# Kernel tuning notes

Hardware: AMD Instinct MI355X
Metric: run time of the kernel (lower is better)

## Reference

```python
import jax, jax.numpy as jnp
import numpy as np

DIM = 1024
NUM_HEADS = 16
HEAD_DIM = DIM // NUM_HEADS
SCALE = HEAD_DIM ** -0.5


def setup_inputs() -> dict:
    key = jax.random.key(0)
    k1, k2, k3 = jax.random.split(key, 3)
    x = jax.random.normal(k1, (4, 2048, DIM), dtype=jnp.float32)
    w_qkv = jax.random.normal(k2, (DIM, 3 * DIM), dtype=jnp.float32) * (DIM ** -0.5)
    b_qkv = jnp.zeros((3 * DIM,), dtype=jnp.float32)
    w_proj = jax.random.normal(k3, (DIM, DIM), dtype=jnp.float32) * (DIM ** -0.5)
    b_proj = jnp.zeros((DIM,), dtype=jnp.float32)
    return {"x": x, "w_qkv": w_qkv, "b_qkv": b_qkv, "w_proj": w_proj, "b_proj": b_proj}


def reference(x, w_qkv, b_qkv, w_proj, b_proj):
    b, n, c = x.shape
    qkv = x @ w_qkv + b_qkv                       # [b, n, 3*dim]
    qkv = qkv.reshape(b, n, 3, NUM_HEADS, HEAD_DIM)
    qkv = jnp.transpose(qkv, (2, 0, 3, 1, 4))     # [3, b, H, n, hd]
    q, k, v = qkv[0], qkv[1], qkv[2]
    attn = jnp.einsum("bhqd,bhkd->bhqk", q, k) * SCALE
    attn = jax.nn.softmax(attn, axis=-1)
    out = jnp.einsum("bhqk,bhkd->bhqd", attn, v)  # [b, H, n, hd]
    out = jnp.transpose(out, (0, 2, 1, 3)).reshape(b, n, c)
    return out @ w_proj + b_proj
```

## Files before the change

### kernel.cpp

```cpp
#include <hip/hip_runtime.h>
#include <hip/hip_bf16.h>

typedef unsigned short u16;
typedef __attribute__((ext_vector_type(8))) short bf16x8;
typedef __attribute__((ext_vector_type(4))) float f32x4;
typedef __attribute__((ext_vector_type(16))) float f32x16;


__device__ __forceinline__ u16 f2bf(float f) {
  union { float f; unsigned u; } v; v.f = f;
  unsigned r = v.u + 0x7fffu + ((v.u >> 16) & 1u);
  return (u16)(r >> 16);
}

#if defined(__has_builtin)
#if __has_builtin(__builtin_amdgcn_cvt_pk_bf16_f32)
#define HAS_PK_BF16 1
#endif
#endif
__device__ __forceinline__ unsigned pk2bf(float a, float b) {
#ifdef HAS_PK_BF16
  typedef __attribute__((ext_vector_type(2))) __bf16 vbf2;
  union { vbf2 v; unsigned u; } u;
  u.v = __builtin_amdgcn_cvt_pk_bf16_f32(a, b);
  return u.u;
#else
  return (unsigned)f2bf(a) | ((unsigned)f2bf(b) << 16);
#endif
}

__device__ __forceinline__ f32x4 mfma16(bf16x8 a, bf16x8 b, f32x4 c) {
  return __builtin_amdgcn_mfma_f32_16x16x32_bf16(a, b, c, 0, 0, 0);
}
__device__ __forceinline__ f32x16 mfma32(bf16x8 a, bf16x8 b, f32x16 c) {
  return __builtin_amdgcn_mfma_f32_32x32x16_bf16(a, b, c, 0, 0, 0);
}

__device__ __forceinline__ void gl_lds16(const void* g, void* l) {
  __builtin_amdgcn_global_load_lds((__attribute__((address_space(1))) void*)g,
                                   (__attribute__((address_space(3))) void*)l,
                                   16, 0, 0);
}

__device__ __forceinline__ void stage128x32(const u16* g0, int ld, u16* lds) {
  const int t = threadIdx.x;
  const int wave = t >> 6;
#pragma unroll
  for (int j = 0; j < 2; ++j) {
    int c = j * 256 + t;
    const u16* gp = g0 + (size_t)(c >> 2) * ld + (c & 3) * 8;
    gl_lds16(gp, lds + (size_t)(j * 256 + wave * 64) * 8);
  }
}


__global__ void cvt_f32_bf16(const float* __restrict__ in, u16* __restrict__ out, int n) {
  int i = (blockIdx.x * blockDim.x + threadIdx.x) * 4;
  if (i >= n) return;
  float4 v = *(const float4*)(in + i);
  u16 o0 = f2bf(v.x), o1 = f2bf(v.y), o2 = f2bf(v.z), o3 = f2bf(v.w);
  ushort4 o; o.x = o0; o.y = o1; o.z = o2; o.w = o3;
  *(ushort4*)(out + i) = o;
}

__global__ void transpose_cvt(const float* __restrict__ in, u16* __restrict__ out,
                              int R, int C) {
  __shared__ u16 tile[64][65];
  int c0 = blockIdx.x * 64, r0 = blockIdx.y * 64;
  int lc = threadIdx.x & 63, lr = threadIdx.x >> 6;
#pragma unroll
  for (int i = 0; i < 16; ++i) {
    int r = lr + i * 4;
    tile[r][lc] = f2bf(in[(size_t)(r0 + r) * C + c0 + lc]);
  }
  __syncthreads();
#pragma unroll
  for (int i = 0; i < 16; ++i) {
    int c = lr + i * 4;
    out[(size_t)(c0 + c) * R + r0 + lc] = tile[lc][c];
  }
}

__global__ void transpose_v(const u16* __restrict__ Vb, u16* __restrict__ Vt) {
  __shared__ u16 tile[64][65];
  int bh = blockIdx.y;
  int s0 = blockIdx.x * 64;
  const u16* in = Vb + (size_t)bh * 2048 * 64;
  u16* out = Vt + (size_t)bh * 64 * 2048;
  int lc = threadIdx.x & 63, lr = threadIdx.x >> 6;
#pragma unroll
  for (int i = 0; i < 16; ++i) {
    int r = lr + i * 4;
    tile[r][lc] = in[(size_t)(s0 + r) * 64 + lc];
  }
  __syncthreads();
#pragma unroll
  for (int i = 0; i < 16; ++i) {
    int d = lr + i * 4;
    out[(size_t)d * 2048 + s0 + lc] = tile[lc][d];
  }
}


__global__ __launch_bounds__(256, 2) void gemm_qkv(
    const u16* __restrict__ A, const u16* __restrict__ Bt,
    const float* __restrict__ bias,
    u16* __restrict__ Qb, u16* __restrict__ Kb, u16* __restrict__ Vb) {
  __shared__ u16 As[128 * 32], Bs[128 * 32];
  const int row0 = blockIdx.x * 128, col0 = blockIdx.y * 128;
  const int t = threadIdx.x, lane = t & 63, wave = t >> 6;
  const int quad = lane >> 4, l15 = lane & 15;
  const int m_off = (wave & 1) * 64, n_off = (wave >> 1) * 64;
  f32x4 acc[4][4] = {};
  for (int k0 = 0; k0 < 1024; k0 += 32) {
    __syncthreads();
    stage128x32(A + (size_t)row0 * 1024 + k0, 1024, As);
    stage128x32(Bt + (size_t)col0 * 1024 + k0, 1024, Bs);
    __syncthreads();
    bf16x8 a[4], b[4];
#pragma unroll
    for (int mi = 0; mi < 4; ++mi)
      a[mi] = *(const bf16x8*)(As + (m_off + mi * 16 + l15) * 32 + quad * 8);
#pragma unroll
    for (int ni = 0; ni < 4; ++ni)
      b[ni] = *(const bf16x8*)(Bs + (n_off + ni * 16 + l15) * 32 + quad * 8);
#pragma unroll
    for (int mi = 0; mi < 4; ++mi)
#pragma unroll
      for (int ni = 0; ni < 4; ++ni)
        acc[mi][ni] = mfma16(a[mi], b[ni], acc[mi][ni]);
  }
  const int which = col0 >> 10;
  u16* dst = which == 0 ? Qb : (which == 1 ? Kb : Vb);
  const float qscale = which == 0 ? 0.1803368801111137f : 1.0f;
#pragma unroll
  for (int ni = 0; ni < 4; ++ni) {
    int col = col0 + n_off + ni * 16 + l15;
    float bv = bias[col];
    int h = (col >> 6) & 15, d = col & 63;
#pragma unroll
    for (int mi = 0; mi < 4; ++mi) {
#pragma unroll
      for (int r = 0; r < 4; ++r) {
        int row = row0 + m_off + mi * 16 + quad * 4 + r;
        int bb = row >> 11, s = row & 2047;
        float v = (acc[mi][ni][r] + bv) * qscale;
        dst[(((size_t)bb * 16 + h) * 2048 + s) * 64 + d] = f2bf(v);
      }
    }
  }
}


__global__ __launch_bounds__(256, 2) void gemm_proj(
    const u16* __restrict__ A, const u16* __restrict__ Bt,
    const float* __restrict__ bias, float* __restrict__ C) {
  __shared__ u16 As[128 * 32], Bs[128 * 32];
  const int row0 = blockIdx.x * 128, col0 = blockIdx.y * 128;
  const int t = threadIdx.x, lane = t & 63, wave = t >> 6;
  const int quad = lane >> 4, l15 = lane & 15;
  const int m_off = (wave & 1) * 64, n_off = (wave >> 1) * 64;
  f32x4 acc[4][4] = {};
  for (int k0 = 0; k0 < 1024; k0 += 32) {
    __syncthreads();
    stage128x32(A + (size_t)row0 * 1024 + k0, 1024, As);
    stage128x32(Bt + (size_t)col0 * 1024 + k0, 1024, Bs);
    __syncthreads();
    bf16x8 a[4], b[4];
#pragma unroll
    for (int mi = 0; mi < 4; ++mi)
      a[mi] = *(const bf16x8*)(As + (m_off + mi * 16 + l15) * 32 + quad * 8);
#pragma unroll
    for (int ni = 0; ni < 4; ++ni)
      b[ni] = *(const bf16x8*)(Bs + (n_off + ni * 16 + l15) * 32 + quad * 8);
#pragma unroll
    for (int mi = 0; mi < 4; ++mi)
#pragma unroll
      for (int ni = 0; ni < 4; ++ni)
        acc[mi][ni] = mfma16(a[mi], b[ni], acc[mi][ni]);
  }
#pragma unroll
  for (int ni = 0; ni < 4; ++ni) {
    int col = col0 + n_off + ni * 16 + l15;
    float bv = bias[col];
#pragma unroll
    for (int mi = 0; mi < 4; ++mi) {
#pragma unroll
      for (int r = 0; r < 4; ++r) {
        int row = row0 + m_off + mi * 16 + quad * 4 + r;
        C[(size_t)row * 1024 + col] = acc[mi][ni][r] + bv;
      }
    }
  }
}


__device__ __forceinline__ void softmax32(const f32x16& s, float& l,
                                          bf16x8& paA, bf16x8& paB) {
  unsigned D[8];
#pragma unroll
  for (int i = 0; i < 8; ++i) {
    float a = __builtin_amdgcn_exp2f(s[2 * i]);
    float b = __builtin_amdgcn_exp2f(s[2 * i + 1]);
    l += a + b;
    D[i] = pk2bf(a, b);
  }
  {
    unsigned x = D[0], x2 = D[1], y = D[2], y2 = D[3];
    asm volatile("v_permlane32_swap_b32 %0, %1" : "+v"(x), "+v"(y));
    asm volatile("v_permlane32_swap_b32 %0, %1" : "+v"(x2), "+v"(y2));
    union { unsigned u[4]; bf16x8 v; } p;
    p.u[0] = x; p.u[1] = x2; p.u[2] = y; p.u[3] = y2;
    paA = p.v;
  }
  {
    unsigned x = D[4], x2 = D[5], y = D[6], y2 = D[7];
    asm volatile("v_permlane32_swap_b32 %0, %1" : "+v"(x), "+v"(y));
    asm volatile("v_permlane32_swap_b32 %0, %1" : "+v"(x2), "+v"(y2));
    union { unsigned u[4]; bf16x8 v; } p;
    p.u[0] = x; p.u[1] = x2; p.u[2] = y; p.u[3] = y2;
    paB = p.v;
  }
}

__global__ __launch_bounds__(256, 2) void attn_kernel(
    const u16* __restrict__ Qb, const u16* __restrict__ Kb,
    const u16* __restrict__ Vt, u16* __restrict__ Ob) {
  __shared__ u16 KsA[64 * 64], KsB[64 * 64];
  __shared__ u16 VsA[64 * 64], VsB[64 * 64];
  const int bh = blockIdx.x, q0 = blockIdx.y * 256;
  const u16* Qp = Qb + (size_t)bh * 2048 * 64;
  const u16* Kp = Kb + (size_t)bh * 2048 * 64;
  const u16* Vp = Vt + (size_t)bh * 64 * 2048;
  const int t = threadIdx.x, lane = t & 63, wave = t >> 6;
  const int l31 = lane & 31, hi = lane >> 5;

  const int kr0 = t >> 3, kc0 = (t & 7) ^ (kr0 & 7);
  const int kr1 = (256 + t) >> 3, kc1 = ((256 + t) & 7) ^ (kr1 & 7);
  const u16* Kg0 = Kp + (size_t)kr0 * 64 + kc0 * 8;
  const u16* Kg1 = Kp + (size_t)kr1 * 64 + kc1 * 8;
  const u16* Vg0 = Vp + (size_t)kr0 * 2048 + kc0 * 8;
  const u16* Vg1 = Vp + (size_t)kr1 * 2048 + kc1 * 8;
  const size_t dof0 = (size_t)wave * 512;
  const size_t dof1 = 2048 + (size_t)wave * 512;

#define STAGE(Kd, Vd, key0)                                   \
  do {                                                        \
    gl_lds16(Kg0 + (size_t)(key0) * 64, (Kd) + dof0);         \
    gl_lds16(Kg1 + (size_t)(key0) * 64, (Kd) + dof1);         \
    gl_lds16(Vg0 + (key0), (Vd) + dof0);                      \
    gl_lds16(Vg1 + (key0), (Vd) + dof1);                      \
  } while (0)

  STAGE(KsA, VsA, 0);
  const u16* Qr0 = Qp + (size_t)(q0 + wave * 64 + l31) * 64 + hi * 8;
  const u16* Qr1 = Qr0 + 32 * 64;
  bf16x8 qf0[4], qf1[4];
#pragma unroll
  for (int dc = 0; dc < 4; ++dc) {
    qf0[dc] = *(const bf16x8*)(Qr0 + dc * 16);
    qf1[dc] = *(const bf16x8*)(Qr1 + dc * 16);
  }
  __syncthreads();

  const int rm = l31 & 7;
  int off[2][4];
#pragma unroll
  for (int x = 0; x < 2; ++x)
#pragma unroll
    for (int c = 0; c < 4; ++c)
      off[x][c] = x * 4096 + l31 * 128 + (((c * 2 + hi) ^ rm) << 4);

  f32x16 acc00 = {}, acc01 = {}, acc10 = {}, acc11 = {};
  float l0 = 0.f, l1 = 0.f;

#define TILE(Ks, Vs)                                                          \
  do {                                                                        \
    _Pragma("unroll")                                                         \
    for (int kh = 0; kh < 2; ++kh) {                                          \
      f32x16 s0 = {}, s1 = {};                                                \
      _Pragma("unroll")                                                       \
      for (int dc = 0; dc < 4; ++dc) {                                        \
        bf16x8 kf = *(const bf16x8*)((const char*)(Ks) + off[kh][dc]);        \
        s0 = mfma32(kf, qf0[dc], s0);                                         \
        s1 = mfma32(kf, qf1[dc], s1);                                         \
      }                                                                       \
      bf16x8 pa00, pa01, pa10, pa11;                                          \
      softmax32(s0, l0, pa00, pa01);                                          \
      softmax32(s1, l1, pa10, pa11);                                          \
      _Pragma("unroll")                                                       \
      for (int ci = 0; ci < 2; ++ci) {                                        \
        const int c = 2 * kh + ci;                                            \
        bf16x8 vlo = *(const bf16x8*)((const char*)(Vs) + off[0][c]);         \
        bf16x8 vhiv = *(const bf16x8*)((const char*)(Vs) + off[1][c]);        \
        bf16x8 pa0 = ci ? pa01 : pa00;                                        \
        bf16x8 pa1 = ci ? pa11 : pa10;                                        \
        acc00 = mfma32(pa0, vlo, acc00);                                      \
        acc01 = mfma32(pa0, vhiv, acc01);                                     \
        acc10 = mfma32(pa1, vlo, acc10);                                      \
        acc11 = mfma32(pa1, vhiv, acc11);                                     \
      }                                                                       \
    }                                                                         \
  } while (0)

#pragma unroll 1
  for (int kt2 = 0; kt2 < 16; ++kt2) {
    const int kt = kt2 * 2;
    STAGE(KsB, VsB, (kt + 1) * 64);
    TILE(KsA, VsA);
    __syncthreads();
    if (kt2 < 15) STAGE(KsA, VsA, (kt + 2) * 64);
    TILE(KsB, VsB);
    __syncthreads();
  }
#undef TILE
#undef STAGE

  l0 += __shfl_xor(l0, 32);
  l1 += __shfl_xor(l1, 32);
  float inv0 = 1.f / l0, inv1 = 1.f / l1;

  const int b_ = bh >> 4, h = bh & 15;
  const int qw = q0 + wave * 64;
#pragma unroll
  for (int r = 0; r < 16; ++r) {
    const int ql = (r & 3) + 8 * (r >> 2) + 4 * hi;
    float iv0 = __shfl(inv0, ql);
    float iv1 = __shfl(inv1, ql);
    size_t base0 = ((size_t)b_ * 2048 + qw + ql) * 1024 + h * 64;
    size_t base1 = base0 + (size_t)32 * 1024;
    Ob[base0 + l31] = f2bf(acc00[r] * iv0);
    Ob[base0 + 32 + l31] = f2bf(acc01[r] * iv0);
    Ob[base1 + l31] = f2bf(acc10[r] * iv1);
    Ob[base1 + 32 + l31] = f2bf(acc11[r] * iv1);
  }
}


extern "C" void kernel_launch(void* const* d_in, const int* in_sizes, int n_in,
                              void* d_out, int out_size, void* d_ws, size_t ws_size,
                              hipStream_t stream) {
  const float* x      = (const float*)d_in[0];
  const float* w_qkv  = (const float*)d_in[1];
  const float* b_qkv  = (const float*)d_in[2];
  const float* w_proj = (const float*)d_in[3];
  const float* b_proj = (const float*)d_in[4];
  float* out = (float*)d_out;
  char* ws = (char*)d_ws;

  u16* xb    = (u16*)(ws);
  u16* wqkvt = (u16*)(ws + 16777216);
  u16* wprjt = (u16*)(ws + 23068672);
  u16* Qb    = (u16*)(ws + 25165824);
  u16* Kb    = (u16*)(ws + 41943040);
  u16* Vb    = (u16*)(ws + 58720256);
  u16* Vt    = (u16*)(ws + 75497472);
  u16* Ob    = xb;
  if (ws_size < 92274688u) return;

  cvt_f32_bf16<<<8192, 256, 0, stream>>>(x, xb, 8388608);
  transpose_cvt<<<dim3(48, 16), 256, 0, stream>>>(w_qkv, wqkvt, 1024, 3072);
  transpose_cvt<<<dim3(16, 16), 256, 0, stream>>>(w_proj, wprjt, 1024, 1024);
  gemm_qkv<<<dim3(64, 24), 256, 0, stream>>>(xb, wqkvt, b_qkv, Qb, Kb, Vb);
  transpose_v<<<dim3(32, 64), 256, 0, stream>>>(Vb, Vt);
  attn_kernel<<<dim3(64, 8), 256, 0, stream>>>(Qb, Kb, Vt, Ob);
  gemm_proj<<<dim3(64, 8), 256, 0, stream>>>(Ob, wprjt, b_proj, out);
}
```

Measured before the change: 278.8 us.

## Fuse V transpose into QKV GEMM epilogue and add MFMA priority hints

The QKV GEMM's V-column blocks now write their output already transposed. They stage the tile through swizzled shared memory and store it with vectorised writes straight into the Vt layout, so the separate transpose_v kernel and its extra global round-trip are removed. The attention inner loop also raises wave priority around the MFMA phases with s_setprio so matrix work is issued ahead of the softmax phases of other waves. The costs are extra shared-memory staging and barriers in the GEMM epilogue for one third of its blocks.

```diff
diff --git a/kernel.cpp b/kernel.cpp
--- a/kernel.cpp
+++ b/kernel.cpp
@@ -81,32 +81,14 @@
   }
 }
 
-__global__ void transpose_v(const u16* __restrict__ Vb, u16* __restrict__ Vt) {
-  __shared__ u16 tile[64][65];
-  int bh = blockIdx.y;
-  int s0 = blockIdx.x * 64;
-  const u16* in = Vb + (size_t)bh * 2048 * 64;
-  u16* out = Vt + (size_t)bh * 64 * 2048;
-  int lc = threadIdx.x & 63, lr = threadIdx.x >> 6;
-#pragma unroll
-  for (int i = 0; i < 16; ++i) {
-    int r = lr + i * 4;
-    tile[r][lc] = in[(size_t)(s0 + r) * 64 + lc];
-  }
-  __syncthreads();
-#pragma unroll
-  for (int i = 0; i < 16; ++i) {
-    int d = lr + i * 4;
-    out[(size_t)d * 2048 + s0 + lc] = tile[lc][d];
-  }
-}
-
 
 __global__ __launch_bounds__(256, 2) void gemm_qkv(
     const u16* __restrict__ A, const u16* __restrict__ Bt,
     const float* __restrict__ bias,
-    u16* __restrict__ Qb, u16* __restrict__ Kb, u16* __restrict__ Vb) {
-  __shared__ u16 As[128 * 32], Bs[128 * 32];
+    u16* __restrict__ Qb, u16* __restrict__ Kb, u16* __restrict__ Vt) {
+  __shared__ u16 smem[128 * 32 * 2];
+  u16* As = smem;
+  u16* Bs = smem + 4096;
   const int row0 = blockIdx.x * 128, col0 = blockIdx.y * 128;
   const int t = threadIdx.x, lane = t & 63, wave = t >> 6;
   const int quad = lane >> 4, l15 = lane & 15;
@@ -131,7 +113,45 @@
         acc[mi][ni] = mfma16(a[mi], b[ni], acc[mi][ni]);
   }
   const int which = col0 >> 10;
-  u16* dst = which == 0 ? Qb : (which == 1 ? Kb : Vb);
+
+  if (which == 2) {
+    u16* Ts = smem;
+    const int h0 = (col0 >> 6) & 15;
+    const int b_ = row0 >> 11;
+    const int s0 = row0 & 2047;
+    const int myp = wave >> 1;
+#pragma unroll
+    for (int p = 0; p < 2; ++p) {
+      __syncthreads();
+      if (myp == p) {
+#pragma unroll
+        for (int ni = 0; ni < 4; ++ni) {
+          const int d = ni * 16 + l15;
+          const float bv = bias[col0 + n_off + ni * 16 + l15];
+#pragma unroll
+          for (int mi = 0; mi < 4; ++mi) {
+            const int sl = m_off + mi * 16 + quad * 4;
+            uint2 pk;
+            pk.x = pk2bf(acc[mi][ni][0] + bv, acc[mi][ni][1] + bv);
+            pk.y = pk2bf(acc[mi][ni][2] + bv, acc[mi][ni][3] + bv);
+            *(uint2*)((char*)Ts + d * 256 + ((2 * sl) ^ ((d & 15) << 4))) = pk;
+          }
+        }
+      }
+      __syncthreads();
+      u16* vt = Vt + ((size_t)(b_ * 16 + h0 + p) * 64) * 2048;
+#pragma unroll
+      for (int k = 0; k < 4; ++k) {
+        int idx = t + 256 * k;
+        int d = idx >> 4, c = idx & 15;
+        uint4 v = *(const uint4*)((const char*)Ts + d * 256 + ((c ^ (d & 15)) << 4));
+        *(uint4*)(vt + (size_t)d * 2048 + s0 + c * 8) = v;
+      }
+    }
+    return;
+  }
+
+  u16* dst = which == 0 ? Qb : Kb;
   const float qscale = which == 0 ? 0.1803368801111137f : 1.0f;
 #pragma unroll
   for (int ni = 0; ni < 4; ++ni) {
@@ -279,15 +299,18 @@
     _Pragma("unroll")                                                         \
     for (int kh = 0; kh < 2; ++kh) {                                          \
       f32x16 s0 = {}, s1 = {};                                                \
+      __builtin_amdgcn_s_setprio(1);                                          \
       _Pragma("unroll")                                                       \
       for (int dc = 0; dc < 4; ++dc) {                                        \
         bf16x8 kf = *(const bf16x8*)((const char*)(Ks) + off[kh][dc]);        \
         s0 = mfma32(kf, qf0[dc], s0);                                         \
         s1 = mfma32(kf, qf1[dc], s1);                                         \
       }                                                                       \
+      __builtin_amdgcn_s_setprio(0);                                          \
       bf16x8 pa00, pa01, pa10, pa11;                                          \
       softmax32(s0, l0, pa00, pa01);                                          \
       softmax32(s1, l1, pa10, pa11);                                          \
+      __builtin_amdgcn_s_setprio(1);                                          \
       _Pragma("unroll")                                                       \
       for (int ci = 0; ci < 2; ++ci) {                                        \
         const int c = 2 * kh + ci;                                            \
@@ -300,6 +323,7 @@
         acc10 = mfma32(pa1, vlo, acc10);                                      \
         acc11 = mfma32(pa1, vhiv, acc11);                                     \
       }                                                                       \
+      __builtin_amdgcn_s_setprio(0);                                          \
     }                                                                         \
   } while (0)
 
@@ -353,16 +377,14 @@
   u16* wprjt = (u16*)(ws + 23068672);
   u16* Qb    = (u16*)(ws + 25165824);
   u16* Kb    = (u16*)(ws + 41943040);
-  u16* Vb    = (u16*)(ws + 58720256);
-  u16* Vt    = (u16*)(ws + 75497472);
+  u16* Vt    = (u16*)(ws + 58720256);
   u16* Ob    = xb;
   if (ws_size < 92274688u) return;
 
   cvt_f32_bf16<<<8192, 256, 0, stream>>>(x, xb, 8388608);
   transpose_cvt<<<dim3(48, 16), 256, 0, stream>>>(w_qkv, wqkvt, 1024, 3072);
   transpose_cvt<<<dim3(16, 16), 256, 0, stream>>>(w_proj, wprjt, 1024, 1024);
-  gemm_qkv<<<dim3(64, 24), 256, 0, stream>>>(xb, wqkvt, b_qkv, Qb, Kb, Vb);
-  transpose_v<<<dim3(32, 64), 256, 0, stream>>>(Vb, Vt);
+  gemm_qkv<<<dim3(64, 24), 256, 0, stream>>>(xb, wqkvt, b_qkv, Qb, Kb, Vt);
   attn_kernel<<<dim3(64, 8), 256, 0, stream>>>(Qb, Kb, Vt, Ob);
   gemm_proj<<<dim3(64, 8), 256, 0, stream>>>(Ob, wprjt, b_proj, out);
 }
```

After: 274.9 us. Within noise of the previous version (-1.4%).
